# Optimization experiments

Measured on AMD Instinct MI355X. Metric: run time of the kernel, lower is better.

## Reference

```python
import jax, jax.numpy as jnp
import numpy as np

K = -1.0          # manifold curvature (hyperbolic / Poincare ball)
SK = 1.0          # sqrt(|K|)
EPS = 1e-7


def _artan_k(x):
    # inverse of tan_k for K<0: artanh(sqrt(|K|) x)/sqrt(|K|)
    return jnp.arctanh(jnp.clip(SK * x, -1.0 + EPS, 1.0 - EPS)) / SK


def _tan_k(x):
    return jnp.tanh(SK * x) / SK


def _norm(x):
    return jnp.maximum(jnp.linalg.norm(x, axis=-1, keepdims=True), 1e-15)


def mobius_add(x, y):
    xy = jnp.sum(x * y, -1, keepdims=True)
    x2 = jnp.sum(x * x, -1, keepdims=True)
    y2 = jnp.sum(y * y, -1, keepdims=True)
    num = (1.0 - 2.0 * K * xy - K * y2) * x + (1.0 + K * x2) * y
    den = 1.0 - 2.0 * K * xy + K * K * x2 * y2
    return num / jnp.maximum(den, 1e-15)


def mobius_scalar_mul(r, x):
    # r may be scalar or (n,1) per-row scalar
    xn = _norm(x)
    return _tan_k(r * _artan_k(xn)) * x / xn


def mobius_matvec(W, x):
    # geoopt convention: (m @ x) per point -> x @ W^T
    xn = _norm(x)
    mx = x @ W.T
    mxn = _norm(mx)
    return _tan_k(mxn / xn * _artan_k(xn)) * mx / mxn


def lambda_x(x):
    # conformal factor lambda_x = 2 / (1 + K |x|^2); returns shape (...,)
    return 2.0 / jnp.maximum(1.0 + K * jnp.sum(x * x, -1), 1e-10)


def expmap0(u):
    un = _norm(u)
    return _tan_k(un) * u / un


def logmap0(y):
    yn = _norm(y)
    return _artan_k(yn) * y / yn


def kappa_left_multiply(A, X):
    # Vectorized per-node weighted gyro-midpoint + mobius scalar mul.
    # out_i = (sum_j A_ij) otimes gyromidpoint(X, weights=A_i)
    gamma = lambda_x(X)                              # (n,)
    denom = A @ (gamma - 1.0)                        # (n,)
    denom = jnp.where(jnp.abs(denom) < 1e-10, 1e-10, denom)
    nom = A @ (gamma[:, None] * X)                   # (n,d)
    two_mean = nom / denom[:, None]
    m = mobius_scalar_mul(0.5, two_mean)             # gyromidpoint
    return mobius_scalar_mul(jnp.sum(A, axis=1, keepdims=True), m)


def setup_inputs() -> dict:
    key = jax.random.key(0)
    k1, k2, k3, k4, k5 = jax.random.split(key, 5)
    n, d, c = 8192, 256, 16
    # node embeddings on the Poincare ball (small norm, well inside the ball)
    X = 0.01 * jax.random.normal(k1, (n, d), jnp.float32)
    # dense normalized adjacency (positive weights, row sums O(1))
    A_hat = jax.random.uniform(k2, (n, n), dtype=jnp.float32) / n
    W = jax.random.uniform(k3, (d, d), dtype=jnp.float32)        # torch.rand init
    W_logits = jax.random.uniform(k4, (d, c), dtype=jnp.float32)
    # p_ks = expmap0(rand), scaled for numerical stability
    p_ks = expmap0(0.05 * jax.random.uniform(k5, (c, d), dtype=jnp.float32))
    return {"X": X, "A_hat": A_hat, "W": W, "W_logits": W_logits, "p_ks": p_ks}


def reference(X, A_hat, W, W_logits, p_ks):
    # hidden kappa-GCN layer
    XW = mobius_matvec(W, X)                          # (n,d)
    AXW = kappa_left_multiply(A_hat, XW)              # (n,d)
    H1 = expmap0(jax.nn.relu(logmap0(AXW)))           # manifold.apply(relu)
    # hyperbolic logits (kappa != 0 branch, K<0 -> asinh)
    z = mobius_add(-p_ks[None, :, :], H1[:, None, :]) # (n,k,d)
    z_n = jnp.linalg.norm(z, axis=-1)                 # (n,k)
    a_n = jnp.maximum(jnp.linalg.norm(W_logits, axis=0), 1e-15)  # (k,)
    za = jnp.einsum('nkd,dk->nk', z, W_logits)
    den = jnp.maximum(1.0 + K * z_n * z_n, 1e-10) * a_n
    dist = jnp.arcsinh(2.0 * SK * za / den)
    lam = lambda_x(p_ks)                              # (k,)
    logits = (lam * a_n / SK) * dist                  # (n,k)
    return A_hat @ logits
```

## Files before the change

### kernel.cpp

```cpp
#include <hip/hip_runtime.h>
#include <math.h>

#define Nn 8192
#define Dd 256
#define Cc 16

#define OFF_BP   4194304u
#define OFF_LOG  5242880u
#define OFF_G1B  5373952u
#define OFF_DEN  5378048u
#define OFF_RS   5410816u
#define OFF_KC   5443584u
#define WS_FLOATS 5443648u

typedef short vshort8 __attribute__((ext_vector_type(8)));
typedef float vfloat4 __attribute__((ext_vector_type(4)));

#define AS1 __attribute__((address_space(1)))
#define AS3 __attribute__((address_space(3)))

__device__ __forceinline__ float clip1(float x) {
    return fminf(fmaxf(x, -1.0f + 1e-7f), 1.0f - 1e-7f);
}

__device__ __forceinline__ unsigned short f2bf(float f) {
    unsigned int u = __float_as_uint(f);
    u += 0x7fff + ((u >> 16) & 1);
    return (unsigned short)(u >> 16);
}

__device__ __forceinline__ float bf2f(unsigned short b) {
    return __uint_as_float(((unsigned int)b) << 16);
}

__device__ __forceinline__ float waveReduce(float v) {
    #pragma unroll
    for (int off = 32; off; off >>= 1) v += __shfl_down(v, off);
    return v;
}

__device__ __forceinline__ float blockReduceBcast(float v, float* red) {
    int t = threadIdx.x, w = t >> 6, l = t & 63;
    v = waveReduce(v);
    if (l == 0) red[w] = v;
    __syncthreads();
    if (t == 0) red[0] = red[0] + red[1] + red[2] + red[3];
    __syncthreads();
    float r = red[0];
    __syncthreads();
    return r;
}

__global__ __launch_bounds__(256) void k_consts(const float* __restrict__ Wl,
                                                const float* __restrict__ Pk,
                                                float* __restrict__ kc) {
    __shared__ float red[8];
    int t = threadIdx.x, k = blockIdx.x;
    float pv = Pk[k * Dd + t];
    float wv = Wl[t * Cc + k];
    float p2 = blockReduceBcast(pv * pv, red);
    float pw = blockReduceBcast(pv * wv, red);
    float w2 = blockReduceBcast(wv * wv, red);
    if (t == 0) {
        float an  = fmaxf(sqrtf(w2), 1e-15f);
        float lam = 2.0f / fmaxf(1.0f - p2, 1e-10f);
        kc[k * 4 + 0] = p2; kc[k * 4 + 1] = pw;
        kc[k * 4 + 2] = an; kc[k * 4 + 3] = lam;
    }
}

__global__ __launch_bounds__(256) void k_front(const float* __restrict__ X,
                                               const float* __restrict__ W,
                                               unsigned short* __restrict__ Bp,
                                               unsigned short* __restrict__ g1b) {
    __shared__ __align__(16) unsigned short Xs[32][256];
    __shared__ __align__(16) unsigned short Gs[32][258];
    __shared__ float xs2[32];
    __shared__ float scal[32];
    __shared__ float red4[32][4];

    const int t = threadIdx.x;
    const int l = t & 63, w = t >> 6;
    const int ll = l & 15, kh = l >> 4;
    const int m0 = blockIdx.x * 32;
    const int ar = t >> 3, aq = t & 7;
    const int c0 = w * 64;

    float x2p = 0.f;
    #pragma unroll
    for (int tc = 0; tc < 4; ++tc) {
        const float* xp = &X[(size_t)(m0 + ar) * Dd + tc * 64 + aq * 8];
        vfloat4 v0 = *(const vfloat4*)xp;
        vfloat4 v1 = *(const vfloat4*)(xp + 4);
        vshort8 o;
        #pragma unroll
        for (int e = 0; e < 4; ++e) {
            x2p += v0[e] * v0[e] + v1[e] * v1[e];
            o[e] = (short)f2bf(v0[e]);
            o[e + 4] = (short)f2bf(v1[e]);
        }
        int byte = (tc * 64 + aq * 8) * 2;
        *(vshort8*)((char*)&Xs[ar][0] + (byte ^ ((ar & 7) << 4))) = o;
    }
    x2p += __shfl_xor(x2p, 1); x2p += __shfl_xor(x2p, 2); x2p += __shfl_xor(x2p, 4);
    if (aq == 0) xs2[ar] = x2p;
    __syncthreads();

    vfloat4 acc[2][4];
    #pragma unroll
    for (int mi = 0; mi < 2; ++mi)
        #pragma unroll
        for (int ni = 0; ni < 4; ++ni)
            acc[mi][ni] = (vfloat4){0.f, 0.f, 0.f, 0.f};
    #pragma unroll
    for (int tc = 0; tc < 4; ++tc) {
        vshort8 bf[8];
        #pragma unroll
        for (int ni = 0; ni < 4; ++ni)
            #pragma unroll
            for (int kk = 0; kk < 2; ++kk) {
                const float* wp = &W[(size_t)(c0 + ni * 16 + ll) * Dd
                                     + tc * 64 + kh * 8 + kk * 32];
                vfloat4 b0 = *(const vfloat4*)wp;
                vfloat4 b1 = *(const vfloat4*)(wp + 4);
                vshort8 o;
                #pragma unroll
                for (int e = 0; e < 4; ++e) {
                    o[e] = (short)f2bf(b0[e]);
                    o[e + 4] = (short)f2bf(b1[e]);
                }
                bf[ni * 2 + kk] = o;
            }
        #pragma unroll
        for (int kk = 0; kk < 2; ++kk) {
            int byte = (tc * 64 + kh * 8 + kk * 32) * 2;
            vshort8 af[2];
            #pragma unroll
            for (int mi = 0; mi < 2; ++mi) {
                int row = mi * 16 + ll;
                af[mi] = *(const vshort8*)((const char*)&Xs[row][0]
                                           + (byte ^ ((row & 7) << 4)));
            }
            #pragma unroll
            for (int mi = 0; mi < 2; ++mi)
                #pragma unroll
                for (int ni = 0; ni < 4; ++ni)
                    acc[mi][ni] = __builtin_amdgcn_mfma_f32_16x16x32_bf16(
                        af[mi], bf[ni * 2 + kk], acc[mi][ni], 0, 0, 0);
        }
    }

    #pragma unroll
    for (int mi = 0; mi < 2; ++mi)
        #pragma unroll
        for (int j = 0; j < 4; ++j) {
            float p = 0.f;
            #pragma unroll
            for (int ni = 0; ni < 4; ++ni)
                p += acc[mi][ni][j] * acc[mi][ni][j];
            p += __shfl_xor(p, 1); p += __shfl_xor(p, 2);
            p += __shfl_xor(p, 4); p += __shfl_xor(p, 8);
            if (ll == 0) red4[mi * 16 + kh * 4 + j][w] = p;
        }
    __syncthreads();

    if (t < 32) {
        float mx2 = red4[t][0] + red4[t][1] + red4[t][2] + red4[t][3];
        float xn = fmaxf(sqrtf(xs2[t]), 1e-15f);
        float mxn = fmaxf(sqrtf(mx2), 1e-15f);
        float s = tanhf(mxn / xn * atanhf(clip1(xn))) / mxn;
        float xw2 = s * s * mx2;
        float gamma = 2.0f / fmaxf(1.0f - xw2, 1e-10f);
        scal[t] = gamma * s;
        g1b[m0 + t] = f2bf(gamma - 1.0f);
    }
    __syncthreads();

    #pragma unroll
    for (int mi = 0; mi < 2; ++mi)
        #pragma unroll
        for (int ni = 0; ni < 4; ++ni) {
            int row = mi * 16 + kh * 4;
            int col = c0 + ni * 16 + ll;
            #pragma unroll
            for (int j = 0; j < 4; ++j)
                Gs[row + j][col] = f2bf(scal[row + j] * acc[mi][ni][j]);
        }
    __syncthreads();

    const int s = blockIdx.x;
    #pragma unroll
    for (int pass = 0; pass < 4; ++pass) {
        int c = pass * 256 + t;
        int gni = c >> 6, lc = c & 63;
        int col = (gni >> 2) * 64 + (gni & 3) * 16 + (lc & 15);
        int kh8 = (lc >> 4) * 8;
        vshort8 o;
        #pragma unroll
        for (int e = 0; e < 8; ++e) o[e] = (short)Gs[kh8 + e][col];
        *(vshort8*)&Bp[((size_t)(s * 16 + gni) * 64 + lc) * 8] = o;
    }
}

__device__ __forceinline__ void g2_issueB(const unsigned short* __restrict__ Bp,
        unsigned short (&BsB)[16][512], int splt, int slab, int w, int l) {
    #pragma unroll
    for (int ni = 0; ni < 4; ++ni)
        __builtin_amdgcn_global_load_lds(
            (const AS1 unsigned int*)
                (Bp + ((size_t)((splt * 64 + slab) * 16 + w * 4 + ni) * 512) + l * 8),
            (AS3 unsigned int*)&BsB[w * 4 + ni][0], 16, 0, 0);
}

__device__ __forceinline__ void g2_loadA(const float* __restrict__ Abase,
                                         int tile, float (&a8)[8]) {
    const vfloat4* p = (const vfloat4*)(Abase + tile * 32);
    *(vfloat4*)&a8[0] = p[0];
    *(vfloat4*)&a8[4] = p[1];
}

__device__ __forceinline__ void g2_stage(unsigned short (&AsB)[2048],
        const unsigned short* g1s, const float (&a8)[8],
        int tile, int rowst, int kq, float& dacc, float& racc) {
    vshort8 gv = *(const vshort8*)&g1s[tile * 32 + kq * 8];
    vshort8 o;
    #pragma unroll
    for (int e = 0; e < 8; ++e) {
        float av = a8[e];
        o[e] = (short)f2bf(av);
        dacc += av * bf2f((unsigned short)gv[e]);
        racc += av;
    }
    *(vshort8*)((char*)&AsB[0] + rowst * 64 + ((kq * 16) ^ ((rowst & 3) << 4))) = o;
}

__device__ __forceinline__ void g2_mfma(const unsigned short (&AsB)[2048],
        const unsigned short (&BsB)[16][512], int w, int kh, int ll15, int l,
        vfloat4 (&acc)[4][4]) {
    vshort8 bf[4], af[4];
    #pragma unroll
    for (int ni = 0; ni < 4; ++ni)
        bf[ni] = *(const vshort8*)&BsB[w * 4 + ni][l * 8];
    #pragma unroll
    for (int mi = 0; mi < 4; ++mi) {
        int row = mi * 16 + ll15;
        af[mi] = *(const vshort8*)((const char*)&AsB[0]
                  + row * 64 + ((kh * 16) ^ ((row & 3) << 4)));
    }
    #pragma unroll
    for (int mi = 0; mi < 4; ++mi)
        #pragma unroll
        for (int ni = 0; ni < 4; ++ni)
            acc[mi][ni] = __builtin_amdgcn_mfma_f32_16x16x32_bf16(
                af[mi], bf[ni], acc[mi][ni], 0, 0, 0);
}

__global__ __launch_bounds__(256, 2) void k_gemm1_mfma(
        const float* __restrict__ A,
        const unsigned short* __restrict__ Bp,
        const unsigned short* __restrict__ g1b,
        unsigned short* __restrict__ Pp,
        float* __restrict__ denp,
        float* __restrict__ rsp) {
    __shared__ __align__(16) unsigned short As[2][2048];
    __shared__ __align__(16) unsigned short Bs[2][16][512];
    __shared__ __align__(16) unsigned short g1s[2048];

    const int t = threadIdx.x, l = t & 63, w = t >> 6;
    const int id = blockIdx.x;
    const int splt = id & 3;
    const int m0 = (id >> 2) * 64;
    const int kb = splt * 2048;
    const int kh = l >> 4, ll15 = l & 15;
    const int rowst = t >> 2, kq = t & 3;

    const float* Abase = &A[(size_t)(m0 + rowst) * Nn + kb + kq * 8];

    vfloat4 acc[4][4];
    #pragma unroll
    for (int mi = 0; mi < 4; ++mi)
        #pragma unroll
        for (int ni = 0; ni < 4; ++ni)
            acc[mi][ni] = (vfloat4){0.f, 0.f, 0.f, 0.f};
    float dacc = 0.f, racc = 0.f;
    float a0[8], a1[8];

    {
        uint4 g1v = *(const uint4*)&g1b[kb + t * 8];
        *(uint4*)&g1s[t * 8] = g1v;
    }
    g2_issueB(Bp, Bs[0], splt, 0, w, l);
    g2_loadA(Abase, 0, a0);
    g2_loadA(Abase, 1, a1);
    asm volatile("s_waitcnt lgkmcnt(0)" ::: "memory");
    __builtin_amdgcn_s_barrier();
    asm volatile("s_waitcnt vmcnt(2)" ::: "memory");
    g2_stage(As[0], g1s, a0, 0, rowst, kq, dacc, racc);
    asm volatile("s_waitcnt lgkmcnt(0)" ::: "memory");
    __builtin_amdgcn_s_barrier();
    __builtin_amdgcn_sched_barrier(0);

    for (int u = 0; u < 31; ++u) {
        const int p = u * 2;
        g2_issueB(Bp, Bs[1], splt, p + 1, w, l);
        g2_loadA(Abase, p + 2, a0);
        asm volatile("s_waitcnt vmcnt(6)" ::: "memory");
        g2_stage(As[1], g1s, a1, p + 1, rowst, kq, dacc, racc);
        g2_mfma(As[0], Bs[0], w, kh, ll15, l, acc);
        asm volatile("s_waitcnt lgkmcnt(0)" ::: "memory");
        __builtin_amdgcn_s_barrier();
        __builtin_amdgcn_sched_barrier(0);
        g2_issueB(Bp, Bs[0], splt, p + 2, w, l);
        g2_loadA(Abase, p + 3, a1);
        asm volatile("s_waitcnt vmcnt(6)" ::: "memory");
        g2_stage(As[0], g1s, a0, p + 2, rowst, kq, dacc, racc);
        g2_mfma(As[1], Bs[1], w, kh, ll15, l, acc);
        asm volatile("s_waitcnt lgkmcnt(0)" ::: "memory");
        __builtin_amdgcn_s_barrier();
        __builtin_amdgcn_sched_barrier(0);
    }
    g2_issueB(Bp, Bs[1], splt, 63, w, l);
    asm volatile("s_waitcnt vmcnt(4)" ::: "memory");
    g2_stage(As[1], g1s, a1, 63, rowst, kq, dacc, racc);
    g2_mfma(As[0], Bs[0], w, kh, ll15, l, acc);
    asm volatile("s_waitcnt lgkmcnt(0)" ::: "memory");
    __builtin_amdgcn_s_barrier();
    __builtin_amdgcn_sched_barrier(0);
    asm volatile("s_waitcnt vmcnt(0)" ::: "memory");
    g2_mfma(As[1], Bs[1], w, kh, ll15, l, acc);

    dacc += __shfl_xor(dacc, 1); dacc += __shfl_xor(dacc, 2);
    racc += __shfl_xor(racc, 1); racc += __shfl_xor(racc, 2);
    if (kq == 0) {
        denp[splt * Nn + m0 + rowst] = dacc;
        rsp [splt * Nn + m0 + rowst] = racc;
    }

    unsigned short* P = Pp + (size_t)splt * ((size_t)Nn * Dd);
    #pragma unroll
    for (int mi = 0; mi < 4; ++mi)
        #pragma unroll
        for (int ni = 0; ni < 4; ++ni) {
            int row = m0 + mi * 16 + (kh << 2);
            int col = w * 64 + ni * 16 + ll15;
            #pragma unroll
            for (int j = 0; j < 4; ++j)
                P[(size_t)(row + j) * Dd + col] = f2bf(acc[mi][ni][j]);
        }
}

__global__ __launch_bounds__(256) void k_rowfix(const unsigned short* __restrict__ Pp,
                                                const float* __restrict__ denp,
                                                const float* __restrict__ rsp,
                                                const float* __restrict__ Pk,
                                                const float* __restrict__ Wl,
                                                const float* __restrict__ kc,
                                                float* __restrict__ logits) {
    __shared__ float red[8];
    __shared__ float hs[256];
    __shared__ float PQ[16][2];
    int i = blockIdx.x, t = threadIdx.x;
    float nom = 0.f;
    #pragma unroll
    for (int s = 0; s < 4; ++s)
        nom += bf2f(Pp[(size_t)s * Nn * Dd + (size_t)i * Dd + t]);
    float dv = denp[i] + denp[Nn + i] + denp[2 * Nn + i] + denp[3 * Nn + i];
    dv = (fabsf(dv) < 1e-10f) ? 1e-10f : dv;
    float tm = nom / dv;
    float r2 = blockReduceBcast(tm * tm, red);
    float r = fmaxf(sqrtf(r2), 1e-15f);
    float mmul = tanhf(0.5f * atanhf(clip1(r))) / r;
    float mj = mmul * tm;
    float mn2 = blockReduceBcast(mj * mj, red);
    float mn = fmaxf(sqrtf(mn2), 1e-15f);
    float sA = rsp[i] + rsp[Nn + i] + rsp[2 * Nn + i] + rsp[3 * Nn + i];
    float axmul = tanhf(sA * atanhf(clip1(mn))) / mn;
    float axw = axmul * mj;
    float yn2 = blockReduceBcast(axw * axw, red);
    float yn = fmaxf(sqrtf(yn2), 1e-15f);
    float v = atanhf(clip1(yn)) / yn * axw;
    float u = fmaxf(v, 0.0f);
    float un2 = blockReduceBcast(u * u, red);
    float un = fmaxf(sqrtf(un2), 1e-15f);
    float h = tanhf(un) / un * u;
    float h2 = blockReduceBcast(h * h, red);
    hs[t] = h;
    __syncthreads();
    int w = t >> 6, l = t & 63;
    #pragma unroll
    for (int kk = 0; kk < 4; ++kk) {
        int k = w * 4 + kk;
        float pp = 0.f, qq = 0.f;
        #pragma unroll
        for (int m = 0; m < 4; ++m) {
            float hv = hs[l + 64 * m];
            pp += hv * Pk[k * Dd + l + 64 * m];
            qq += hv * Wl[(l + 64 * m) * Cc + k];
        }
        pp = waveReduce(pp);
        qq = waveReduce(qq);
        if (l == 0) { PQ[k][0] = pp; PQ[k][1] = qq; }
    }
    __syncthreads();
    if (t < 16) {
        int k = t;
        float p2 = kc[k * 4 + 0], pw = kc[k * 4 + 1];
        float an = kc[k * 4 + 2], lam = kc[k * 4 + 3];
        float P = PQ[k][0], Q = PQ[k][1];
        float alpha = 1.0f - 2.0f * P + h2;
        float beta  = 1.0f - p2;
        float Dm = fmaxf(1.0f - 2.0f * P + p2 * h2, 1e-15f);
        float za  = (-alpha * pw + beta * Q) / Dm;
        float zn2 = (alpha * alpha * p2 - 2.0f * alpha * beta * P + beta * beta * h2)
                    / (Dm * Dm);
        float dd = fmaxf(1.0f - zn2, 1e-10f) * an;
        float dist = asinhf(2.0f * za / dd);
        logits[(size_t)i * Cc + k] = lam * an * dist;
    }
}

__global__ __launch_bounds__(256) void k_gemm2(const float* __restrict__ A,
                                               const float* __restrict__ L,
                                               float* __restrict__ part) {
    __shared__ __align__(16) float Ls[64 * 20];
    __shared__ float Pacc[256 * 16];
    int t = threadIdx.x;
    int r0 = blockIdx.x * 256;
    int jbase = blockIdx.y * 512;
    int q = t & 3, g = t >> 2;
    float acc[4][16] = {};
    for (int jc = 0; jc < 512; jc += 64) {
        {
            int jrow = t >> 2, kq2 = t & 3;
            *(float4*)&Ls[jrow * 20 + kq2 * 4] =
                *(const float4*)&L[(size_t)(jbase + jc + jrow) * Cc + kq2 * 4];
        }
        __syncthreads();
        #pragma unroll
        for (int m = 0; m < 4; ++m) {
            int jl = m * 16 + q * 4;
            float av[4][4];
            #pragma unroll
            for (int rr = 0; rr < 4; ++rr) {
                float4 tmp = *(const float4*)&A[(size_t)(r0 + g * 4 + rr) * Nn
                                                + jbase + jc + jl];
                av[rr][0] = tmp.x; av[rr][1] = tmp.y;
                av[rr][2] = tmp.z; av[rr][3] = tmp.w;
            }
            #pragma unroll
            for (int jj = 0; jj < 4; ++jj) {
                const float* lr = &Ls[(jl + jj) * 20];
                float lv[16];
                #pragma unroll
                for (int k2 = 0; k2 < 16; k2 += 4) {
                    float4 lt = *(const float4*)&lr[k2];
                    lv[k2] = lt.x; lv[k2 + 1] = lt.y;
                    lv[k2 + 2] = lt.z; lv[k2 + 3] = lt.w;
                }
                #pragma unroll
                for (int rr = 0; rr < 4; ++rr)
                    #pragma unroll
                    for (int k2 = 0; k2 < 16; ++k2)
                        acc[rr][k2] += av[rr][jj] * lv[k2];
            }
        }
        __syncthreads();
    }
    for (int ii = t; ii < 4096; ii += 256) Pacc[ii] = 0.f;
    __syncthreads();
    for (int qq = 0; qq < 4; ++qq) {
        if (q == qq) {
            #pragma unroll
            for (int rr = 0; rr < 4; ++rr)
                #pragma unroll
                for (int k2 = 0; k2 < 16; ++k2)
                    Pacc[(g * 4 + rr) * 16 + k2] += acc[rr][k2];
        }
        __syncthreads();
    }
    float* dst = &part[(size_t)blockIdx.y * (Nn * Cc) + (size_t)r0 * Cc];
    for (int ii = t * 4; ii < 4096; ii += 1024)
        *(float4*)&dst[ii] = *(const float4*)&Pacc[ii];
}

__global__ __launch_bounds__(256) void k_reduce(const float* __restrict__ part,
                                                float* __restrict__ out) {
    int i = blockIdx.x * 256 + threadIdx.x;
    float s = 0.f;
    #pragma unroll
    for (int j = 0; j < 16; ++j) s += part[(size_t)j * (Nn * Cc) + i];
    out[i] = s;
}

extern "C" void kernel_launch(void* const* d_in, const int* in_sizes, int n_in,
                              void* d_out, int out_size, void* d_ws, size_t ws_size,
                              hipStream_t stream) {
    const float* X  = (const float*)d_in[0];
    const float* A  = (const float*)d_in[1];
    const float* W  = (const float*)d_in[2];
    const float* Wl = (const float*)d_in[3];
    const float* Pk = (const float*)d_in[4];
    float* out = (float*)d_out;
    float* ws = (float*)d_ws;
    if (ws_size < (size_t)WS_FLOATS * sizeof(float)) return;

    unsigned short* Pp  = (unsigned short*)ws;
    float* part = ws;
    unsigned short* Bp  = (unsigned short*)(ws + OFF_BP);
    float* lg   = ws + OFF_LOG;
    unsigned short* g1b = (unsigned short*)(ws + OFF_G1B);
    float* denp = ws + OFF_DEN;
    float* rsp  = ws + OFF_RS;
    float* kc   = ws + OFF_KC;

    k_consts<<<16, 256, 0, stream>>>(Wl, Pk, kc);
    k_front<<<256, 256, 0, stream>>>(X, W, Bp, g1b);
    k_gemm1_mfma<<<512, 256, 0, stream>>>(A, Bp, g1b, Pp, denp, rsp);
    k_rowfix<<<Nn, 256, 0, stream>>>(Pp, denp, rsp, Pk, Wl, kc, lg);
    k_gemm2<<<dim3(32, 16), 256, 0, stream>>>(A, lg, part);
    k_reduce<<<512, 256, 0, stream>>>(part, out);
}
```

Measured before the change: 220.4 us.

## Deepen gemm1 prefetch pipeline to four stages and raise MFMA wave priority

The big A_hat GEMM kernel now keeps four B tiles and four A register tiles in flight instead of two, with a uniform 4-way unrolled loop. It also wraps the MFMA block in s_setprio so matrix-issuing waves get scheduling priority. The aim is to hide more global-memory latency on the dominant streaming of A_hat. In exchange it uses more LDS (which may reduce occupancy below 2 blocks/CU), more registers, and issues redundant wrapped-around loads in the tail iterations.

```diff
diff --git a/kernel.cpp b/kernel.cpp
--- a/kernel.cpp
+++ b/kernel.cpp
@@ -247,12 +247,14 @@
         af[mi] = *(const vshort8*)((const char*)&AsB[0]
                   + row * 64 + ((kh * 16) ^ ((row & 3) << 4)));
     }
+    __builtin_amdgcn_s_setprio(1);
     #pragma unroll
     for (int mi = 0; mi < 4; ++mi)
         #pragma unroll
         for (int ni = 0; ni < 4; ++ni)
             acc[mi][ni] = __builtin_amdgcn_mfma_f32_16x16x32_bf16(
                 af[mi], bf[ni], acc[mi][ni], 0, 0, 0);
+    __builtin_amdgcn_s_setprio(0);
 }
 
 __global__ __launch_bounds__(256, 2) void k_gemm1_mfma(
@@ -263,7 +265,7 @@
         float* __restrict__ denp,
         float* __restrict__ rsp) {
     __shared__ __align__(16) unsigned short As[2][2048];
-    __shared__ __align__(16) unsigned short Bs[2][16][512];
+    __shared__ __align__(16) unsigned short Bs[4][16][512];
     __shared__ __align__(16) unsigned short g1s[2048];
 
     const int t = threadIdx.x, l = t & 63, w = t >> 6;
@@ -283,51 +285,47 @@
         for (int ni = 0; ni < 4; ++ni)
             acc[mi][ni] = (vfloat4){0.f, 0.f, 0.f, 0.f};
     float dacc = 0.f, racc = 0.f;
-    float a0[8], a1[8];
-
-    {
-        uint4 g1v = *(const uint4*)&g1b[kb + t * 8];
-        *(uint4*)&g1s[t * 8] = g1v;
-    }
+    float a0[8], a1[8], a2[8], a3[8];
+
+    uint4 g1v = *(const uint4*)&g1b[kb + t * 8];
     g2_issueB(Bp, Bs[0], splt, 0, w, l);
+    g2_issueB(Bp, Bs[1], splt, 1, w, l);
+    g2_issueB(Bp, Bs[2], splt, 2, w, l);
     g2_loadA(Abase, 0, a0);
     g2_loadA(Abase, 1, a1);
+    g2_loadA(Abase, 2, a2);
+    g2_loadA(Abase, 3, a3);
+    asm volatile("s_waitcnt vmcnt(0)" ::: "memory");
+    *(uint4*)&g1s[t * 8] = g1v;
     asm volatile("s_waitcnt lgkmcnt(0)" ::: "memory");
     __builtin_amdgcn_s_barrier();
-    asm volatile("s_waitcnt vmcnt(2)" ::: "memory");
     g2_stage(As[0], g1s, a0, 0, rowst, kq, dacc, racc);
     asm volatile("s_waitcnt lgkmcnt(0)" ::: "memory");
     __builtin_amdgcn_s_barrier();
     __builtin_amdgcn_sched_barrier(0);
 
-    for (int u = 0; u < 31; ++u) {
-        const int p = u * 2;
-        g2_issueB(Bp, Bs[1], splt, p + 1, w, l);
-        g2_loadA(Abase, p + 2, a0);
-        asm volatile("s_waitcnt vmcnt(6)" ::: "memory");
-        g2_stage(As[1], g1s, a1, p + 1, rowst, kq, dacc, racc);
-        g2_mfma(As[0], Bs[0], w, kh, ll15, l, acc);
-        asm volatile("s_waitcnt lgkmcnt(0)" ::: "memory");
-        __builtin_amdgcn_s_barrier();
-        __builtin_amdgcn_sched_barrier(0);
-        g2_issueB(Bp, Bs[0], splt, p + 2, w, l);
-        g2_loadA(Abase, p + 3, a1);
-        asm volatile("s_waitcnt vmcnt(6)" ::: "memory");
-        g2_stage(As[0], g1s, a0, p + 2, rowst, kq, dacc, racc);
-        g2_mfma(As[1], Bs[1], w, kh, ll15, l, acc);
-        asm volatile("s_waitcnt lgkmcnt(0)" ::: "memory");
-        __builtin_amdgcn_s_barrier();
-        __builtin_amdgcn_sched_barrier(0);
-    }
-    g2_issueB(Bp, Bs[1], splt, 63, w, l);
-    asm volatile("s_waitcnt vmcnt(4)" ::: "memory");
-    g2_stage(As[1], g1s, a1, 63, rowst, kq, dacc, racc);
-    g2_mfma(As[0], Bs[0], w, kh, ll15, l, acc);
-    asm volatile("s_waitcnt lgkmcnt(0)" ::: "memory");
-    __builtin_amdgcn_s_barrier();
-    __builtin_amdgcn_sched_barrier(0);
-    asm volatile("s_waitcnt vmcnt(0)" ::: "memory");
-    g2_mfma(As[1], Bs[1], w, kh, ll15, l, acc);
+    for (int u = 0; u < 16; ++u) {
+        #pragma unroll
+        for (int pp = 0; pp < 4; ++pp) {
+            const int q = u * 4 + pp;
+            g2_issueB(Bp, Bs[(pp + 3) & 3], splt, (q + 3) & 63, w, l);
+            {
+                float (&adst)[8] = (pp == 0) ? a0 : (pp == 1) ? a1
+                                 : (pp == 2) ? a2 : a3;
+                g2_loadA(Abase, (q + 4) & 63, adst);
+            }
+            asm volatile("s_waitcnt vmcnt(18)" ::: "memory");
+            if (q < 63) {
+                float (&asrc)[8] = (pp == 0) ? a1 : (pp == 1) ? a2
+                                 : (pp == 2) ? a3 : a0;
+                g2_stage(As[(q + 1) & 1], g1s, asrc, q + 1, rowst, kq, dacc, racc);
+            }
+            g2_mfma(As[q & 1], Bs[pp & 3], w, kh, ll15, l, acc);
+            asm volatile("s_waitcnt lgkmcnt(0)" ::: "memory");
+            __builtin_amdgcn_s_barrier();
+            __builtin_amdgcn_sched_barrier(0);
+        }
+    }
 
     dacc += __shfl_xor(dacc, 1); dacc += __shfl_xor(dacc, 2);
     racc += __shfl_xor(racc, 1); racc += __shfl_xor(racc, 2);
```

New measurement: 212.8 us. -3.5%, faster.

## Halve gemm1 M-tile to 32 rows, deepen A prefetch, raise occupancy

Applied to the files above, without the earlier changes.

The A×(XW) MFMA GEMM now processes 32 rows per block instead of 64, which doubles the grid to 1024 blocks and raises the launch bound to 4 blocks per CU. A loads become 4 floats per thread, prefetched three tiles ahead and rotated through four register buffers. MFMA issue is wrapped in s_setprio to favour compute waves. The aim is more parallelism and better latency hiding on the A stream, at the cost of re-reading B twice as often and a lower ratio of MFMA work to loads per block.

```diff
diff --git a/kernel.cpp b/kernel.cpp
--- a/kernel.cpp
+++ b/kernel.cpp
@@ -14,6 +14,7 @@
 #define WS_FLOATS 5443648u
 
 typedef short vshort8 __attribute__((ext_vector_type(8)));
+typedef short vshort4 __attribute__((ext_vector_type(4)));
 typedef float vfloat4 __attribute__((ext_vector_type(4)));
 
 #define AS1 __attribute__((address_space(1)))
@@ -213,115 +214,132 @@
 }
 
 __device__ __forceinline__ void g2_loadA(const float* __restrict__ Abase,
-                                         int tile, float (&a8)[8]) {
-    const vfloat4* p = (const vfloat4*)(Abase + tile * 32);
-    *(vfloat4*)&a8[0] = p[0];
-    *(vfloat4*)&a8[4] = p[1];
-}
-
-__device__ __forceinline__ void g2_stage(unsigned short (&AsB)[2048],
-        const unsigned short* g1s, const float (&a8)[8],
+                                         int tile, float (&a4)[4]) {
+    *(vfloat4*)&a4[0] = *(const vfloat4*)(Abase + tile * 32);
+}
+
+__device__ __forceinline__ void g2_stage(unsigned short (&AsB)[1024],
+        const unsigned short* g1s, const float (&a4)[4],
         int tile, int rowst, int kq, float& dacc, float& racc) {
-    vshort8 gv = *(const vshort8*)&g1s[tile * 32 + kq * 8];
-    vshort8 o;
-    #pragma unroll
-    for (int e = 0; e < 8; ++e) {
-        float av = a8[e];
+    vshort4 gv = *(const vshort4*)&g1s[tile * 32 + kq * 4];
+    vshort4 o;
+    #pragma unroll
+    for (int e = 0; e < 4; ++e) {
+        float av = a4[e];
         o[e] = (short)f2bf(av);
         dacc += av * bf2f((unsigned short)gv[e]);
         racc += av;
     }
-    *(vshort8*)((char*)&AsB[0] + rowst * 64 + ((kq * 16) ^ ((rowst & 3) << 4))) = o;
-}
-
-__device__ __forceinline__ void g2_mfma(const unsigned short (&AsB)[2048],
+    *(vshort4*)((char*)&AsB[0] + rowst * 64 + ((kq * 8) ^ ((rowst & 3) << 4))) = o;
+}
+
+__device__ __forceinline__ void g2_mfma(const unsigned short (&AsB)[1024],
         const unsigned short (&BsB)[16][512], int w, int kh, int ll15, int l,
-        vfloat4 (&acc)[4][4]) {
-    vshort8 bf[4], af[4];
+        vfloat4 (&acc)[2][4]) {
+    vshort8 bf[4], af[2];
     #pragma unroll
     for (int ni = 0; ni < 4; ++ni)
         bf[ni] = *(const vshort8*)&BsB[w * 4 + ni][l * 8];
     #pragma unroll
-    for (int mi = 0; mi < 4; ++mi) {
+    for (int mi = 0; mi < 2; ++mi) {
         int row = mi * 16 + ll15;
         af[mi] = *(const vshort8*)((const char*)&AsB[0]
                   + row * 64 + ((kh * 16) ^ ((row & 3) << 4)));
     }
-    #pragma unroll
-    for (int mi = 0; mi < 4; ++mi)
+    __builtin_amdgcn_s_setprio(1);
+    #pragma unroll
+    for (int mi = 0; mi < 2; ++mi)
         #pragma unroll
         for (int ni = 0; ni < 4; ++ni)
             acc[mi][ni] = __builtin_amdgcn_mfma_f32_16x16x32_bf16(
                 af[mi], bf[ni], acc[mi][ni], 0, 0, 0);
-}
-
-__global__ __launch_bounds__(256, 2) void k_gemm1_mfma(
+    __builtin_amdgcn_s_setprio(0);
+}
+
+__global__ __launch_bounds__(256, 4) void k_gemm1_mfma(
         const float* __restrict__ A,
         const unsigned short* __restrict__ Bp,
         const unsigned short* __restrict__ g1b,
         unsigned short* __restrict__ Pp,
         float* __restrict__ denp,
         float* __restrict__ rsp) {
-    __shared__ __align__(16) unsigned short As[2][2048];
+    __shared__ __align__(16) unsigned short As[2][1024];
     __shared__ __align__(16) unsigned short Bs[2][16][512];
     __shared__ __align__(16) unsigned short g1s[2048];
 
     const int t = threadIdx.x, l = t & 63, w = t >> 6;
     const int id = blockIdx.x;
     const int splt = id & 3;
-    const int m0 = (id >> 2) * 64;
+    const int m0 = (id >> 2) * 32;
     const int kb = splt * 2048;
     const int kh = l >> 4, ll15 = l & 15;
-    const int rowst = t >> 2, kq = t & 3;
-
-    const float* Abase = &A[(size_t)(m0 + rowst) * Nn + kb + kq * 8];
-
-    vfloat4 acc[4][4];
-    #pragma unroll
-    for (int mi = 0; mi < 4; ++mi)
+    const int rowst = t >> 3, kq = t & 7;
+
+    const float* Abase = &A[(size_t)(m0 + rowst) * Nn + kb + kq * 4];
+
+    vfloat4 acc[2][4];
+    #pragma unroll
+    for (int mi = 0; mi < 2; ++mi)
         #pragma unroll
         for (int ni = 0; ni < 4; ++ni)
             acc[mi][ni] = (vfloat4){0.f, 0.f, 0.f, 0.f};
     float dacc = 0.f, racc = 0.f;
-    float a0[8], a1[8];
-
-    {
-        uint4 g1v = *(const uint4*)&g1b[kb + t * 8];
-        *(uint4*)&g1s[t * 8] = g1v;
-    }
+    float a0[4], a1[4], a2[4], a3[4];
+
+    uint4 g1v = *(const uint4*)&g1b[kb + t * 8];
     g2_issueB(Bp, Bs[0], splt, 0, w, l);
     g2_loadA(Abase, 0, a0);
     g2_loadA(Abase, 1, a1);
+    g2_loadA(Abase, 2, a2);
+    asm volatile("s_waitcnt vmcnt(0)" ::: "memory");
+    *(uint4*)&g1s[t * 8] = g1v;
     asm volatile("s_waitcnt lgkmcnt(0)" ::: "memory");
     __builtin_amdgcn_s_barrier();
-    asm volatile("s_waitcnt vmcnt(2)" ::: "memory");
     g2_stage(As[0], g1s, a0, 0, rowst, kq, dacc, racc);
     asm volatile("s_waitcnt lgkmcnt(0)" ::: "memory");
     __builtin_amdgcn_s_barrier();
     __builtin_amdgcn_sched_barrier(0);
 
-    for (int u = 0; u < 31; ++u) {
-        const int p = u * 2;
-        g2_issueB(Bp, Bs[1], splt, p + 1, w, l);
-        g2_loadA(Abase, p + 2, a0);
-        asm volatile("s_waitcnt vmcnt(6)" ::: "memory");
-        g2_stage(As[1], g1s, a1, p + 1, rowst, kq, dacc, racc);
-        g2_mfma(As[0], Bs[0], w, kh, ll15, l, acc);
-        asm volatile("s_waitcnt lgkmcnt(0)" ::: "memory");
-        __builtin_amdgcn_s_barrier();
-        __builtin_amdgcn_sched_barrier(0);
-        g2_issueB(Bp, Bs[0], splt, p + 2, w, l);
-        g2_loadA(Abase, p + 3, a1);
-        asm volatile("s_waitcnt vmcnt(6)" ::: "memory");
-        g2_stage(As[0], g1s, a0, p + 2, rowst, kq, dacc, racc);
-        g2_mfma(As[1], Bs[1], w, kh, ll15, l, acc);
-        asm volatile("s_waitcnt lgkmcnt(0)" ::: "memory");
-        __builtin_amdgcn_s_barrier();
-        __builtin_amdgcn_sched_barrier(0);
-    }
+    for (int u = 0; u < 15; ++u) {
+        #pragma unroll
+        for (int pp = 0; pp < 4; ++pp) {
+            const int q = u * 4 + pp;
+            g2_issueB(Bp, Bs[(q + 1) & 1], splt, q + 1, w, l);
+            {
+                float (&adst)[4] = (pp == 0) ? a3 : (pp == 1) ? a0
+                                 : (pp == 2) ? a1 : a2;
+                g2_loadA(Abase, q + 3, adst);
+            }
+            asm volatile("s_waitcnt vmcnt(6)" ::: "memory");
+            {
+                float (&asrc)[4] = (pp == 0) ? a1 : (pp == 1) ? a2
+                                 : (pp == 2) ? a3 : a0;
+                g2_stage(As[(q + 1) & 1], g1s, asrc, q + 1, rowst, kq, dacc, racc);
+            }
+            g2_mfma(As[q & 1], Bs[q & 1], w, kh, ll15, l, acc);
+            asm volatile("s_waitcnt lgkmcnt(0)" ::: "memory");
+            __builtin_amdgcn_s_barrier();
+            __builtin_amdgcn_sched_barrier(0);
+        }
+    }
+    g2_issueB(Bp, Bs[1], splt, 61, w, l);
+    g2_loadA(Abase, 63, a3);
+    asm volatile("s_waitcnt vmcnt(6)" ::: "memory");
+    g2_stage(As[1], g1s, a1, 61, rowst, kq, dacc, racc);
+    g2_mfma(As[0], Bs[0], w, kh, ll15, l, acc);
+    asm volatile("s_waitcnt lgkmcnt(0)" ::: "memory");
+    __builtin_amdgcn_s_barrier();
+    __builtin_amdgcn_sched_barrier(0);
+    g2_issueB(Bp, Bs[0], splt, 62, w, l);
+    asm volatile("s_waitcnt vmcnt(5)" ::: "memory");
+    g2_stage(As[0], g1s, a2, 62, rowst, kq, dacc, racc);
+    g2_mfma(As[1], Bs[1], w, kh, ll15, l, acc);
+    asm volatile("s_waitcnt lgkmcnt(0)" ::: "memory");
+    __builtin_amdgcn_s_barrier();
+    __builtin_amdgcn_sched_barrier(0);
     g2_issueB(Bp, Bs[1], splt, 63, w, l);
     asm volatile("s_waitcnt vmcnt(4)" ::: "memory");
-    g2_stage(As[1], g1s, a1, 63, rowst, kq, dacc, racc);
+    g2_stage(As[1], g1s, a3, 63, rowst, kq, dacc, racc);
     g2_mfma(As[0], Bs[0], w, kh, ll15, l, acc);
     asm volatile("s_waitcnt lgkmcnt(0)" ::: "memory");
     __builtin_amdgcn_s_barrier();
@@ -329,8 +347,8 @@
     asm volatile("s_waitcnt vmcnt(0)" ::: "memory");
     g2_mfma(As[1], Bs[1], w, kh, ll15, l, acc);
 
-    dacc += __shfl_xor(dacc, 1); dacc += __shfl_xor(dacc, 2);
-    racc += __shfl_xor(racc, 1); racc += __shfl_xor(racc, 2);
+    dacc += __shfl_xor(dacc, 1); dacc += __shfl_xor(dacc, 2); dacc += __shfl_xor(dacc, 4);
+    racc += __shfl_xor(racc, 1); racc += __shfl_xor(racc, 2); racc += __shfl_xor(racc, 4);
     if (kq == 0) {
         denp[splt * Nn + m0 + rowst] = dacc;
         rsp [splt * Nn + m0 + rowst] = racc;
@@ -338,7 +356,7 @@
 
     unsigned short* P = Pp + (size_t)splt * ((size_t)Nn * Dd);
     #pragma unroll
-    for (int mi = 0; mi < 4; ++mi)
+    for (int mi = 0; mi < 2; ++mi)
         #pragma unroll
         for (int ni = 0; ni < 4; ++ni) {
             int row = m0 + mi * 16 + (kh << 2);
@@ -515,7 +533,7 @@
 
     k_consts<<<16, 256, 0, stream>>>(Wl, Pk, kc);
     k_front<<<256, 256, 0, stream>>>(X, W, Bp, g1b);
-    k_gemm1_mfma<<<512, 256, 0, stream>>>(A, Bp, g1b, Pp, denp, rsp);
+    k_gemm1_mfma<<<1024, 256, 0, stream>>>(A, Bp, g1b, Pp, denp, rsp);
     k_rowfix<<<Nn, 256, 0, stream>>>(Pp, denp, rsp, Pk, Wl, kc, lg);
     k_gemm2<<<dim3(32, 16), 256, 0, stream>>>(A, lg, part);
     k_reduce<<<512, 256, 0, stream>>>(part, out);
```

Result: slower. 239.1 us (+8.5%).
